# Optimization experiments

Hardware: AMD Instinct MI355X
Metric: run time of the kernel (lower is better)

The kernel has to match this reference:

```python
import jax, jax.numpy as jnp
import numpy as np

N = 4096

def setup_inputs() -> dict:
    key = jax.random.key(0)
    kA, kB = jax.random.split(key)
    A = jnp.tril(jax.random.normal(kA, (N, N), dtype=jnp.float32))
    B = jnp.tril(jax.random.normal(kB, (N, N), dtype=jnp.float32))
    return {"A": A, "B": B}

def reference(A, B):
    # Product of two lower-triangular matrices; result is lower-triangular.
    # tril applied to the dense matmul reproduces the intended math exactly
    # (and zeroes any numerical noise in the structural-zero upper triangle).
    return jnp.tril(jnp.matmul(A, B))
```

## Files before the change

kernel.cpp:

```cpp
#include <hip/hip_runtime.h>
#include <stdint.h>

#define NN 4096
#define NB 32
#define BK 64

#define NHUNITS 272
#define ZBASE 664
#define TGRID 1160

#define PGRID 8328

typedef __bf16 bf16x8 __attribute__((ext_vector_type(8)));
typedef float f32x4 __attribute__((ext_vector_type(4)));
typedef unsigned short ushort8 __attribute__((ext_vector_type(8)));

__device__ __forceinline__ unsigned short f2bf(float x) {
    union { float f; unsigned int u; } v; v.f = x;
    unsigned int u = v.u;
    u += 0x7fffu + ((u >> 16) & 1u);
    return (unsigned short)(u >> 16);
}

#define GLOAD16(g, l) __builtin_amdgcn_global_load_lds( \
    (const __attribute__((address_space(1))) unsigned int*)(g), \
    (__attribute__((address_space(3))) unsigned int*)(l), 16, 0, 0)

__device__ __forceinline__ void heavy_map(int h, int& bi, int& bj) {
    int t = h, d = NB - 1;
    while (t >= NB - d) { t -= NB - d; --d; }
    bj = t; bi = t + d;
}

__global__ __launch_bounds__(256) void prep(const float* __restrict__ A,
                                            const float* __restrict__ B,
                                            unsigned short* __restrict__ Ab,
                                            unsigned short* __restrict__ Bt,
                                            float* __restrict__ C) {
    __shared__ float tile[64][65];
    int bid = blockIdx.x;
    int tid = threadIdx.x;

    if (bid < 4096) {
        int i = bid;
        int nslots = (((i >> 7) + 1) * 128) >> 3;
        const float4* src = reinterpret_cast<const float4*>(A + (size_t)i * NN);
        unsigned short* dst = Ab + (size_t)i * NN;
        for (int p = tid; p < nslots; p += 256) {
            float4 x0 = src[p * 2], x1 = src[p * 2 + 1];
            ushort8 o;
            o[0] = f2bf(x0.x); o[1] = f2bf(x0.y); o[2] = f2bf(x0.z); o[3] = f2bf(x0.w);
            o[4] = f2bf(x1.x); o[5] = f2bf(x1.y); o[6] = f2bf(x1.z); o[7] = f2bf(x1.w);
            *reinterpret_cast<ushort8*>(dst + p * 8) = o;
        }
        return;
    }
    if (bid < 8192) {
        int s = bid - 4096;
        int n64 = s >> 6, k64 = s & 63;
        if (k64 < (n64 & ~1)) return;
        int n0 = n64 * 64, k0 = k64 * 64;
        int tx = tid & 63, ty = tid >> 6;
#pragma unroll
        for (int r = 0; r < 16; ++r) {
            int k = ty + r * 4;
            tile[k][tx] = B[(size_t)(k0 + k) * NN + n0 + tx];
        }
        __syncthreads();
#pragma unroll
        for (int r = 0; r < 16; ++r) {
            int n = ty + r * 4;
            Bt[(size_t)(n0 + n) * NN + k0 + tx] = f2bf(tile[tx][n]);
        }
        return;
    }
    int h = bid - 8192;
    int bi, bj; heavy_map(h, bi, bj);
    float4 z = make_float4(0.f, 0.f, 0.f, 0.f);
    float4* cp = reinterpret_cast<float4*>(C + (size_t)bi * 128 * NN + (size_t)bj * 128);
#pragma unroll
    for (int i2 = 0; i2 < 16; ++i2) {
        int slot = tid + i2 * 256;
        int row = slot >> 5, c4 = slot & 31;
        cp[(size_t)row * (NN / 4) + c4] = z;
    }
}

__global__ __launch_bounds__(256, 2) void trimm(const unsigned short* __restrict__ Ab,
                                                const unsigned short* __restrict__ Bt,
                                                float* __restrict__ C) {
    int bid = blockIdx.x;
    int tid = threadIdx.x;
    int lane = tid & 63;
    int w = tid >> 6;

    int bi, bj;
    bool heavy = false;
    int k_lo, k_hi;

    if (bid >= ZBASE) {
        int t = bid - ZBASE;
        int r = 0, cnt = NB - 1;
        while (t >= cnt) { t -= cnt; ++r; --cnt; }
        bi = r; bj = r + 1 + t;
        float4 z = make_float4(0.f, 0.f, 0.f, 0.f);
        float4* cp = reinterpret_cast<float4*>(C + (size_t)bi * 128 * NN + (size_t)bj * 128);
#pragma unroll
        for (int i2 = 0; i2 < 16; ++i2) {
            int slot = tid + i2 * 256;
            int row = slot >> 5, c4 = slot & 31;
            cp[(size_t)row * (NN / 4) + c4] = z;
        }
        return;
    }
    if (bid < NHUNITS) {
        heavy = true;
        int h = bid >> 1, half = bid & 1;
        heavy_map(h, bi, bj);
        k_lo = bj * 128;
        k_hi = (bi + 1) * 128;
        int len = (k_hi - k_lo) >> 1;
        if (half == 0) k_hi = k_lo + len;
        else           k_lo = k_lo + len;
    } else {
        int t = bid - NHUNITS, d = 15;
        while (t >= NB - d) { t -= NB - d; --d; }
        bj = t; bi = t + d;
        k_lo = bj * 128;
        k_hi = (bi + 1) * 128;
    }

    __shared__ unsigned short As[2][128 * BK];
    __shared__ unsigned short Bs[2][128 * BK];

    int wr = w >> 1, wc = w & 1;

    int srow = tid >> 3;
    int schunk = ((tid & 7) ^ (srow & 7)) * 8;
    const unsigned short* gA = Ab + (size_t)(bi * 128 + srow) * NN + schunk;
    const unsigned short* gB = Bt + (size_t)(bj * 128 + srow) * NN + schunk;

    f32x4 acc[4][4];
#pragma unroll
    for (int mi = 0; mi < 4; ++mi)
#pragma unroll
        for (int ni = 0; ni < 4; ++ni)
            acc[mi][ni] = (f32x4){0.f, 0.f, 0.f, 0.f};

    int fr = lane & 15;
    int c0 = (((lane >> 4) ^ (lane & 7)) * 8);
    int c1 = ((((lane >> 4) | 4) ^ (lane & 7)) * 8);
    int arow = wr * 64 + fr;
    int brow = wc * 64 + fr;

#define STAGE(bufsel, kk) do { \
        unsigned short* la_ = &As[bufsel][0] + tid * 8; \
        unsigned short* lb_ = &Bs[bufsel][0] + tid * 8; \
        GLOAD16(gA + (kk), la_); \
        GLOAD16(gA + (kk) + (size_t)32 * NN, la_ + 2048); \
        GLOAD16(gA + (kk) + (size_t)64 * NN, la_ + 4096); \
        GLOAD16(gA + (kk) + (size_t)96 * NN, la_ + 6144); \
        GLOAD16(gB + (kk), lb_); \
        GLOAD16(gB + (kk) + (size_t)32 * NN, lb_ + 2048); \
        GLOAD16(gB + (kk) + (size_t)64 * NN, lb_ + 4096); \
        GLOAD16(gB + (kk) + (size_t)96 * NN, lb_ + 6144); \
    } while (0)

    int nt = (k_hi - k_lo) >> 6;

    STAGE(0, k_lo);
    STAGE(1, k_lo + BK);
    int cur = 0;

    for (int t = 0; t < nt; ++t) {
        asm volatile("s_waitcnt vmcnt(8)" ::: "memory");
        __builtin_amdgcn_s_barrier();

        const unsigned short* Ac = &As[cur][0];
        const unsigned short* Bc = &Bs[cur][0];
        bf16x8 a0[4], a1[4], b0[4], b1[4];
#pragma unroll
        for (int m = 0; m < 4; ++m) {
            a0[m] = *reinterpret_cast<const bf16x8*>(&Ac[(arow + m * 16) * BK + c0]);
            a1[m] = *reinterpret_cast<const bf16x8*>(&Ac[(arow + m * 16) * BK + c1]);
        }
#pragma unroll
        for (int n = 0; n < 4; ++n) {
            b0[n] = *reinterpret_cast<const bf16x8*>(&Bc[(brow + n * 16) * BK + c0]);
            b1[n] = *reinterpret_cast<const bf16x8*>(&Bc[(brow + n * 16) * BK + c1]);
        }
#pragma unroll
        for (int m = 0; m < 4; ++m)
#pragma unroll
            for (int n = 0; n < 4; ++n) {
                acc[m][n] = __builtin_amdgcn_mfma_f32_16x16x32_bf16(a0[m], b0[n], acc[m][n], 0, 0, 0);
                acc[m][n] = __builtin_amdgcn_mfma_f32_16x16x32_bf16(a1[m], b1[n], acc[m][n], 0, 0, 0);
            }

        __builtin_amdgcn_s_barrier();

        int kn = k_lo + (t + 2) * BK;
        if (kn >= k_hi) kn = k_lo;
        STAGE(cur, kn);

        cur ^= 1;
    }
    asm volatile("s_waitcnt vmcnt(0)" ::: "memory");
#undef STAGE

    int crow0 = bi * 128 + wr * 64 + (lane >> 4) * 4;
    int ccol0 = bj * 128 + wc * 64 + fr;
    if (heavy) {
#pragma unroll
        for (int mi = 0; mi < 4; ++mi)
#pragma unroll
            for (int ni = 0; ni < 4; ++ni) {
                float* cp = C + (size_t)(crow0 + mi * 16) * NN + ccol0 + ni * 16;
#pragma unroll
                for (int r2 = 0; r2 < 4; ++r2)
                    atomicAdd(&cp[(size_t)r2 * NN], acc[mi][ni][r2]);
            }
    } else {
#pragma unroll
        for (int mi = 0; mi < 4; ++mi)
#pragma unroll
            for (int ni = 0; ni < 4; ++ni) {
                float* cp = C + (size_t)(crow0 + mi * 16) * NN + ccol0 + ni * 16;
#pragma unroll
                for (int r2 = 0; r2 < 4; ++r2)
                    cp[(size_t)r2 * NN] = acc[mi][ni][r2];
            }
    }
}

extern "C" void kernel_launch(void* const* d_in, const int* in_sizes, int n_in,
                              void* d_out, int out_size, void* d_ws, size_t ws_size,
                              hipStream_t stream) {
    const float* A = (const float*)d_in[0];
    const float* B = (const float*)d_in[1];
    float* C = (float*)d_out;
    unsigned short* Ab = (unsigned short*)d_ws;
    unsigned short* Bt = Ab + (size_t)NN * NN;
    prep<<<PGRID, 256, 0, stream>>>(A, B, Ab, Bt, C);
    trimm<<<TGRID, 256, 0, stream>>>(Ab, Bt, C);
}
```

Measured before the change: 75.68 us.

## Split-K all lower tiles into balanced units with at most fourteen K-steps

Replaces the fixed two-way split of the 136 longest diagonal tiles with a general split-K scheme: each lower-triangular tile is divided into ceil((d+14)/14) parts so every work unit does roughly at most 28 K-iterations, with atomics used whenever a tile is split. Prep now zeroes every split tile (35 more) before accumulation. This aims to balance load across the CUs and shorten the tail, in exchange for more atomic traffic and more zeroing. It also raises wave priority around the MFMA block with s_setprio.

```diff
diff --git a/kernel.cpp b/kernel.cpp
--- a/kernel.cpp
+++ b/kernel.cpp
@@ -5,11 +5,11 @@
 #define NB 32
 #define BK 64
 
-#define NHUNITS 272
-#define ZBASE 664
-#define TGRID 1160
-
-#define PGRID 8328
+#define NUNITS 709
+#define ZBASE 709
+#define TGRID 1205
+
+#define PGRID 8363
 
 typedef __bf16 bf16x8 __attribute__((ext_vector_type(8)));
 typedef float f32x4 __attribute__((ext_vector_type(4)));
@@ -25,12 +25,6 @@
 #define GLOAD16(g, l) __builtin_amdgcn_global_load_lds( \
     (const __attribute__((address_space(1))) unsigned int*)(g), \
     (__attribute__((address_space(3))) unsigned int*)(l), 16, 0, 0)
-
-__device__ __forceinline__ void heavy_map(int h, int& bi, int& bj) {
-    int t = h, d = NB - 1;
-    while (t >= NB - d) { t -= NB - d; --d; }
-    bj = t; bi = t + d;
-}
 
 __global__ __launch_bounds__(256) void prep(const float* __restrict__ A,
                                             const float* __restrict__ B,
@@ -74,15 +68,22 @@
         }
         return;
     }
-    int h = bid - 8192;
-    int bi, bj; heavy_map(h, bi, bj);
-    float4 z = make_float4(0.f, 0.f, 0.f, 0.f);
-    float4* cp = reinterpret_cast<float4*>(C + (size_t)bi * 128 * NN + (size_t)bj * 128);
-#pragma unroll
-    for (int i2 = 0; i2 < 16; ++i2) {
-        int slot = tid + i2 * 256;
-        int row = slot >> 5, c4 = slot & 31;
-        cp[(size_t)row * (NN / 4) + c4] = z;
+    {
+        int z = bid - 8192;
+        int d = NB - 1, bi, bj;
+        for (;;) {
+            int cnt = NB - d;
+            if (z < cnt) { bj = z; bi = z + d; break; }
+            z -= cnt; --d;
+        }
+        float4 zf = make_float4(0.f, 0.f, 0.f, 0.f);
+        float4* cp = reinterpret_cast<float4*>(C + (size_t)bi * 128 * NN + (size_t)bj * 128);
+#pragma unroll
+        for (int i2 = 0; i2 < 16; ++i2) {
+            int slot = tid + i2 * 256;
+            int row = slot >> 5, c4 = slot & 31;
+            cp[(size_t)row * (NN / 4) + c4] = zf;
+        }
     }
 }
 
@@ -94,15 +95,11 @@
     int lane = tid & 63;
     int w = tid >> 6;
 
-    int bi, bj;
-    bool heavy = false;
-    int k_lo, k_hi;
-
     if (bid >= ZBASE) {
         int t = bid - ZBASE;
         int r = 0, cnt = NB - 1;
         while (t >= cnt) { t -= cnt; ++r; --cnt; }
-        bi = r; bj = r + 1 + t;
+        int bi = r, bj = r + 1 + t;
         float4 z = make_float4(0.f, 0.f, 0.f, 0.f);
         float4* cp = reinterpret_cast<float4*>(C + (size_t)bi * 128 * NN + (size_t)bj * 128);
 #pragma unroll
@@ -113,22 +110,27 @@
         }
         return;
     }
-    if (bid < NHUNITS) {
-        heavy = true;
-        int h = bid >> 1, half = bid & 1;
-        heavy_map(h, bi, bj);
-        k_lo = bj * 128;
-        k_hi = (bi + 1) * 128;
-        int len = (k_hi - k_lo) >> 1;
-        if (half == 0) k_hi = k_lo + len;
-        else           k_lo = k_lo + len;
-    } else {
-        int t = bid - NHUNITS, d = 15;
-        while (t >= NB - d) { t -= NB - d; --d; }
+
+    int bi, bj, k_lo, nt;
+    bool atom;
+    {
+        int r = bid, d = NB - 1, nu;
+        for (;;) {
+            nu = (d + 14) / 14;
+            int cnt = (NB - d) * nu;
+            if (r < cnt) break;
+            r -= cnt; --d;
+        }
+        int t = r / nu, part = r - t * nu;
         bj = t; bi = t + d;
-        k_lo = bj * 128;
-        k_hi = (bi + 1) * 128;
-    }
+        atom = (nu > 1);
+        int ntk = 2 * (d + 1);
+        int ntb = ntk / nu, rem = ntk % nu;
+        nt = ntb + (part < rem ? 1 : 0);
+        int skip = part * ntb + (part < rem ? part : rem);
+        k_lo = bj * 128 + skip * BK;
+    }
+    int k_hi = k_lo + nt * BK;
 
     __shared__ unsigned short As[2][128 * BK];
     __shared__ unsigned short Bs[2][128 * BK];
@@ -166,8 +168,6 @@
         GLOAD16(gB + (kk) + (size_t)96 * NN, lb_ + 6144); \
     } while (0)
 
-    int nt = (k_hi - k_lo) >> 6;
-
     STAGE(0, k_lo);
     STAGE(1, k_lo + BK);
     int cur = 0;
@@ -189,6 +189,7 @@
             b0[n] = *reinterpret_cast<const bf16x8*>(&Bc[(brow + n * 16) * BK + c0]);
             b1[n] = *reinterpret_cast<const bf16x8*>(&Bc[(brow + n * 16) * BK + c1]);
         }
+        __builtin_amdgcn_s_setprio(1);
 #pragma unroll
         for (int m = 0; m < 4; ++m)
 #pragma unroll
@@ -196,6 +197,7 @@
                 acc[m][n] = __builtin_amdgcn_mfma_f32_16x16x32_bf16(a0[m], b0[n], acc[m][n], 0, 0, 0);
                 acc[m][n] = __builtin_amdgcn_mfma_f32_16x16x32_bf16(a1[m], b1[n], acc[m][n], 0, 0, 0);
             }
+        __builtin_amdgcn_s_setprio(0);
 
         __builtin_amdgcn_s_barrier();
 
@@ -210,7 +212,7 @@
 
     int crow0 = bi * 128 + wr * 64 + (lane >> 4) * 4;
     int ccol0 = bj * 128 + wc * 64 + fr;
-    if (heavy) {
+    if (atom) {
 #pragma unroll
         for (int mi = 0; mi < 4; ++mi)
 #pragma unroll
```

Measured after the change: 81.52 us. 1.08x slower.

## Replace split-K atomics with workspace partials and a merge kernel, raise MFMA priority

Applied to the files above, without the earlier changes.

Heavy tiles split along K no longer zero C in prep and atomically add into it. The first half stores directly to C, the second half writes its partial tile to a workspace buffer, and a new merge kernel adds the two. This removes the per-element float atomics and the prep-time zeroing of heavy tiles, at the cost of an extra kernel launch and an extra read/write pass over those tiles. The change also wraps the MFMA block in s_setprio to favour the math waves.

```diff
diff --git a/kernel.cpp b/kernel.cpp
--- a/kernel.cpp
+++ b/kernel.cpp
@@ -5,11 +5,13 @@
 #define NB 32
 #define BK 64
 
+#define NHEAVY 136
 #define NHUNITS 272
 #define ZBASE 664
 #define TGRID 1160
 
-#define PGRID 8328
+#define PGRID_W 8192
+#define PGRID_A 8328
 
 typedef __bf16 bf16x8 __attribute__((ext_vector_type(8)));
 typedef float f32x4 __attribute__((ext_vector_type(4)));
@@ -88,21 +90,19 @@
 
 __global__ __launch_bounds__(256, 2) void trimm(const unsigned short* __restrict__ Ab,
                                                 const unsigned short* __restrict__ Bt,
-                                                float* __restrict__ C) {
+                                                float* __restrict__ C,
+                                                float* __restrict__ W,
+                                                int useW) {
     int bid = blockIdx.x;
     int tid = threadIdx.x;
     int lane = tid & 63;
     int w = tid >> 6;
 
-    int bi, bj;
-    bool heavy = false;
-    int k_lo, k_hi;
-
     if (bid >= ZBASE) {
         int t = bid - ZBASE;
         int r = 0, cnt = NB - 1;
         while (t >= cnt) { t -= cnt; ++r; --cnt; }
-        bi = r; bj = r + 1 + t;
+        int bi = r, bj = r + 1 + t;
         float4 z = make_float4(0.f, 0.f, 0.f, 0.f);
         float4* cp = reinterpret_cast<float4*>(C + (size_t)bi * 128 * NN + (size_t)bj * 128);
 #pragma unroll
@@ -113,9 +113,15 @@
         }
         return;
     }
+
+    int bi, bj;
+    bool heavy = false;
+    int h = 0, half = 0;
+    int k_lo, k_hi;
+
     if (bid < NHUNITS) {
         heavy = true;
-        int h = bid >> 1, half = bid & 1;
+        h = bid >> 1; half = bid & 1;
         heavy_map(h, bi, bj);
         k_lo = bj * 128;
         k_hi = (bi + 1) * 128;
@@ -189,6 +195,7 @@
             b0[n] = *reinterpret_cast<const bf16x8*>(&Bc[(brow + n * 16) * BK + c0]);
             b1[n] = *reinterpret_cast<const bf16x8*>(&Bc[(brow + n * 16) * BK + c1]);
         }
+        __builtin_amdgcn_s_setprio(1);
 #pragma unroll
         for (int m = 0; m < 4; ++m)
 #pragma unroll
@@ -196,6 +203,7 @@
                 acc[m][n] = __builtin_amdgcn_mfma_f32_16x16x32_bf16(a0[m], b0[n], acc[m][n], 0, 0, 0);
                 acc[m][n] = __builtin_amdgcn_mfma_f32_16x16x32_bf16(a1[m], b1[n], acc[m][n], 0, 0, 0);
             }
+        __builtin_amdgcn_s_setprio(0);
 
         __builtin_amdgcn_s_barrier();
 
@@ -208,9 +216,34 @@
     asm volatile("s_waitcnt vmcnt(0)" ::: "memory");
 #undef STAGE
 
-    int crow0 = bi * 128 + wr * 64 + (lane >> 4) * 4;
-    int ccol0 = bj * 128 + wc * 64 + fr;
-    if (heavy) {
+    int trow0 = wr * 64 + (lane >> 4) * 4;
+    int tcol0 = wc * 64 + fr;
+    int crow0 = bi * 128 + trow0;
+    int ccol0 = bj * 128 + tcol0;
+    if (heavy && useW) {
+        if (half == 1) {
+            float* wb = W + (size_t)h * 16384;
+#pragma unroll
+            for (int mi = 0; mi < 4; ++mi)
+#pragma unroll
+                for (int ni = 0; ni < 4; ++ni) {
+                    float* wp = wb + (size_t)(trow0 + mi * 16) * 128 + tcol0 + ni * 16;
+#pragma unroll
+                    for (int r2 = 0; r2 < 4; ++r2)
+                        wp[r2 * 128] = acc[mi][ni][r2];
+                }
+        } else {
+#pragma unroll
+            for (int mi = 0; mi < 4; ++mi)
+#pragma unroll
+                for (int ni = 0; ni < 4; ++ni) {
+                    float* cp = C + (size_t)(crow0 + mi * 16) * NN + ccol0 + ni * 16;
+#pragma unroll
+                    for (int r2 = 0; r2 < 4; ++r2)
+                        cp[(size_t)r2 * NN] = acc[mi][ni][r2];
+                }
+        }
+    } else if (heavy) {
 #pragma unroll
         for (int mi = 0; mi < 4; ++mi)
 #pragma unroll
@@ -230,6 +263,24 @@
                 for (int r2 = 0; r2 < 4; ++r2)
                     cp[(size_t)r2 * NN] = acc[mi][ni][r2];
             }
+    }
+}
+
+__global__ __launch_bounds__(256) void merge(const float* __restrict__ W,
+                                             float* __restrict__ C) {
+    int h = blockIdx.x;
+    int tid = threadIdx.x;
+    int bi, bj; heavy_map(h, bi, bj);
+    const float4* wv = reinterpret_cast<const float4*>(W + (size_t)h * 16384);
+    float4* cp = reinterpret_cast<float4*>(C + (size_t)bi * 128 * NN + (size_t)bj * 128);
+#pragma unroll
+    for (int i2 = 0; i2 < 16; ++i2) {
+        int slot = tid + i2 * 256;
+        int row = slot >> 5, c4 = slot & 31;
+        float4 a = cp[(size_t)row * (NN / 4) + c4];
+        float4 b = wv[slot];
+        a.x += b.x; a.y += b.y; a.z += b.z; a.w += b.w;
+        cp[(size_t)row * (NN / 4) + c4] = a;
     }
 }
 
@@ -241,6 +292,12 @@
     float* C = (float*)d_out;
     unsigned short* Ab = (unsigned short*)d_ws;
     unsigned short* Bt = Ab + (size_t)NN * NN;
-    prep<<<PGRID, 256, 0, stream>>>(A, B, Ab, Bt, C);
-    trimm<<<TGRID, 256, 0, stream>>>(Ab, Bt, C);
-}
+    const size_t base = (size_t)2 * NN * NN * sizeof(unsigned short);
+    const size_t wbytes = (size_t)NHEAVY * 16384 * sizeof(float);
+    const int useW = (ws_size >= base + wbytes) ? 1 : 0;
+    float* W = (float*)((char*)d_ws + base);
+
+    prep<<<useW ? PGRID_W : PGRID_A, 256, 0, stream>>>(A, B, Ab, Bt, C);
+    trimm<<<TGRID, 256, 0, stream>>>(Ab, Bt, C, W, useW);
+    if (useW) merge<<<NHEAVY, 256, 0, stream>>>(W, C);
+}
```

Measured after the change: 82.73 us. +9.3%, slower.

## Remap compute blocks into balanced per-XCD row groups and raise MFMA priority

Applied to the files above, without the earlier changes.

Replaces the linear heavy/light tile ordering with a mapping keyed on bid&7. Each group of 8 interleaved blocks, presumably one per XCD, receives a paired set of block-rows (31-x with 16+x, 15-x with x), so the triangular work is spread evenly across XCDs and L2 reuse of A rows improves. Heavy tiles in those rows are still split along K and accumulated with atomics. It also wraps the MFMA loop in s_setprio(1)/s_setprio(0) so waves doing math are favoured over waves issuing loads. The remapping adds more index arithmetic per block and relies on assumptions about how blocks are assigned to XCDs.

```diff
diff --git a/kernel.cpp b/kernel.cpp
--- a/kernel.cpp
+++ b/kernel.cpp
@@ -5,7 +5,7 @@
 #define NB 32
 #define BK 64
 
-#define NHUNITS 272
+#define NCOMP 664
 #define ZBASE 664
 #define TGRID 1160
 
@@ -94,15 +94,11 @@
     int lane = tid & 63;
     int w = tid >> 6;
 
-    int bi, bj;
-    bool heavy = false;
-    int k_lo, k_hi;
-
     if (bid >= ZBASE) {
         int t = bid - ZBASE;
         int r = 0, cnt = NB - 1;
         while (t >= cnt) { t -= cnt; ++r; --cnt; }
-        bi = r; bj = r + 1 + t;
+        int bi = r, bj = r + 1 + t;
         float4 z = make_float4(0.f, 0.f, 0.f, 0.f);
         float4* cp = reinterpret_cast<float4*>(C + (size_t)bi * 128 * NN + (size_t)bj * 128);
 #pragma unroll
@@ -113,21 +109,41 @@
         }
         return;
     }
-    if (bid < NHUNITS) {
-        heavy = true;
-        int h = bid >> 1, half = bid & 1;
-        heavy_map(h, bi, bj);
-        k_lo = bj * 128;
-        k_hi = (bi + 1) * 128;
-        int len = (k_hi - k_lo) >> 1;
-        if (half == 0) k_hi = k_lo + len;
-        else           k_lo = k_lo + len;
-    } else {
-        int t = bid - NHUNITS, d = 15;
-        while (t >= NB - d) { t -= NB - d; --d; }
-        bj = t; bi = t + d;
-        k_lo = bj * 128;
-        k_hi = (bi + 1) * 128;
+
+    int bi, bj;
+    bool heavy = false;
+    int k_lo, k_hi;
+    {
+        int x = bid & 7, s = bid >> 3;
+        int rA = 31 - x, rB = 16 + x, rC = 15 - x, rD = x;
+        int nHA = 2 * (16 - x);
+        int nHB = 2 * (x + 1);
+        int d;
+        if (s < nHA) {
+            heavy = true;
+            int p = s >> 1, half = s & 1;
+            bi = rA; d = rA - p; bj = p;
+            int base = bj * 128, len = (d + 1) * 64;
+            k_lo = base + (half ? len : 0);
+            k_hi = k_lo + len;
+        } else if (s < nHA + nHB) {
+            heavy = true;
+            int i = s - nHA;
+            int p = i >> 1, half = i & 1;
+            bi = rB; d = rB - p; bj = p;
+            int base = bj * 128, len = (d + 1) * 64;
+            k_lo = base + (half ? len : 0);
+            k_hi = k_lo + len;
+        } else {
+            int i = s - nHA - nHB;
+            if (i < 16)            { bi = rA; d = 15 - i; }
+            else if (i < 32)       { bi = rB; d = 15 - (i - 16); }
+            else if (i < 48 - x)   { bi = rC; d = rC - (i - 32); }
+            else                   { bi = rD; d = rD - (i - (48 - x)); }
+            bj = bi - d;
+            k_lo = bj * 128;
+            k_hi = (bi + 1) * 128;
+        }
     }
 
     __shared__ unsigned short As[2][128 * BK];
@@ -189,6 +205,7 @@
             b0[n] = *reinterpret_cast<const bf16x8*>(&Bc[(brow + n * 16) * BK + c0]);
             b1[n] = *reinterpret_cast<const bf16x8*>(&Bc[(brow + n * 16) * BK + c1]);
         }
+        __builtin_amdgcn_s_setprio(1);
 #pragma unroll
         for (int m = 0; m < 4; ++m)
 #pragma unroll
@@ -196,6 +213,7 @@
                 acc[m][n] = __builtin_amdgcn_mfma_f32_16x16x32_bf16(a0[m], b0[n], acc[m][n], 0, 0, 0);
                 acc[m][n] = __builtin_amdgcn_mfma_f32_16x16x32_bf16(a1[m], b1[n], acc[m][n], 0, 0, 0);
             }
+        __builtin_amdgcn_s_setprio(0);
 
         __builtin_amdgcn_s_barrier();
 
```

After: 75.21 us. No clear change (-0.6%).
